# Kernel optimization log

Measured on AMD Instinct MI355X. Metric: run time of the kernel, lower is better.

Reference implementation:

```python
import jax, jax.numpy as jnp
import numpy as np

HEADS = 8
KEY_DIM = 64
GROUPS = 16
EPS = 1e-5


def setup_inputs() -> dict:
    key = jax.random.key(0)
    ks = jax.random.split(key, 7)
    b, c, h, w = 4, 256, 128, 128
    dk = KEY_DIM * HEADS  # 512
    x = jax.random.normal(ks[0], (b, c, h, w), dtype=jnp.float32)
    wq = jax.random.normal(ks[1], (dk, c), dtype=jnp.float32) * 0.02      # to_q (1x1, no bias)
    wkv = jax.random.normal(ks[2], (2 * dk, c), dtype=jnp.float32) * 0.02  # to_kv (1x1, no bias)
    wo = jax.random.normal(ks[3], (c, dk), dtype=jnp.float32) * 0.02       # to_out weight (1x1)
    bo = jax.random.normal(ks[4], (c,), dtype=jnp.float32) * 0.02          # to_out bias
    gamma = jnp.ones((2 * c,), dtype=jnp.float32)                          # GroupNorm weight
    beta = jnp.zeros((2 * c,), dtype=jnp.float32)                          # GroupNorm bias
    return {"x": x, "wq": wq, "wkv": wkv, "wo": wo, "bo": bo, "gamma": gamma, "beta": beta}


def reference(x, wq, wkv, wo, bo, gamma, beta):
    b, c, h, w = x.shape
    n = h * w
    xf = x.reshape(b, c, n)

    # 1x1 conv projections == channel GEMMs
    q = jnp.einsum('dc,bcn->bdn', wq, xf).reshape(b, HEADS, KEY_DIM, n)
    kv = jnp.einsum('dc,bcn->bdn', wkv, xf)
    k, v = jnp.split(kv, 2, axis=1)
    k = k.reshape(b, HEADS, KEY_DIM, n)
    v = v.reshape(b, HEADS, KEY_DIM, n)

    scale = KEY_DIM ** (-0.25)
    k = jax.nn.softmax(k * scale, axis=-1)   # softmax over spatial n
    q = jax.nn.softmax(q * scale, axis=-2)   # norm_queries: softmax over key_dim

    ctx = jnp.einsum('bhdn,bhen->bhde', k, v)   # [b,h,64,64]
    out = jnp.einsum('bhdn,bhde->bhen', q, ctx)  # [b,h,64,n]
    out = out.reshape(b, HEADS * KEY_DIM, n)

    out = jnp.einsum('od,bdn->bon', wo, out) + bo[None, :, None]  # to_out 1x1 conv

    y = jnp.concatenate([out, xf], axis=1)  # [b, 2c, n]
    c2 = 2 * c
    yg = y.reshape(b, GROUPS, (c2 // GROUPS) * n)
    mean = yg.mean(axis=2, keepdims=True)
    var = yg.var(axis=2, keepdims=True)
    yn = ((yg - mean) * jax.lax.rsqrt(var + EPS)).reshape(b, c2, n)
    yn = yn * gamma[None, :, None] + beta[None, :, None]
    return yn.reshape(b, c2, h, w)
```

## Files before the change

kernel.cpp:

```cpp
#include <hip/hip_runtime.h>

typedef int    i32x4 __attribute__((ext_vector_type(4)));
typedef float  f32x4 __attribute__((ext_vector_type(4)));
typedef __bf16 bf16x8 __attribute__((ext_vector_type(8)));
union B16 { i32x4 i; bf16x8 v; };

#define NN 16384
#define QSCALE 0.35355339059327373f
#define EPSV 1e-5f
#define GRPN 524288.0f

#define GSUM_OFF 0
#define GSQ_OFF  64
#define WS_ZERO_FLOATS 128


__device__ __forceinline__ ushort f2bfu(float f) {
  union { __bf16 h; ushort u; } c; c.h = (__bf16)f; return c.u;
}
__device__ __forceinline__ uint packbf2(float lo, float hi) {
  return (uint)f2bfu(lo) | ((uint)f2bfu(hi) << 16);
}
__device__ __forceinline__ void gload_lds16(const void* g, void* l) {
  __builtin_amdgcn_global_load_lds(
      (const __attribute__((address_space(1))) void*)g,
      (__attribute__((address_space(3))) void*)l, 16, 0, 0);
}

__global__ __launch_bounds__(256) void k_cvt3(const float* __restrict__ a,
                                              const float* __restrict__ bsrc,
                                              const float* __restrict__ c,
                                              ushort* __restrict__ d) {
  int i = (blockIdx.x * 256 + threadIdx.x) * 4;
  const float* s; int off;
  if (i < 131072)      { s = a;    off = 0; }
  else if (i < 393216) { s = bsrc; off = 131072; }
  else                 { s = c;    off = 393216; }
  float4 v = *(const float4*)(s + (i - off));
  uint2 p; p.x = packbf2(v.x, v.y); p.y = packbf2(v.z, v.w);
  *(uint2*)(d + i) = p;
}

__global__ __launch_bounds__(256) void k0_xprep(const float* __restrict__ x,
                                                float* __restrict__ outp,
                                                float* ws) {
  const int t = threadIdx.x;
  const int n0 = blockIdx.x * 64, b = blockIdx.z;
  __shared__ __align__(16) uint tile[64 * 130];
  const int cl = t >> 3;
  const int nb = (t & 7) * 8;
  const bool even = ((t >> 3) & 1) == 0;
  const int cpl = t >> 4;

  float4 va[8][2];
  #pragma unroll
  for (int cg = 0; cg < 8; ++cg) {
    const float* src = x + ((size_t)(b * 256 + cg * 32 + cl)) * NN + n0 + nb;
    va[cg][0] = *(const float4*)src;
    va[cg][1] = *(const float4*)(src + 4);
  }

  float s[8], s2[8];
  #pragma unroll
  for (int g = 0; g < 8; ++g) { s[g] = 0.f; s2[g] = 0.f; }

  #pragma unroll
  for (int cg = 0; cg < 8; ++cg) {
    float v[8] = {va[cg][0].x, va[cg][0].y, va[cg][0].z, va[cg][0].w,
                  va[cg][1].x, va[cg][1].y, va[cg][1].z, va[cg][1].w};
    #pragma unroll
    for (int j = 0; j < 8; ++j) { s[cg] += v[j]; s2[cg] += v[j] * v[j]; }
    float th[8];
    #pragma unroll
    for (int j = 0; j < 8; ++j) th[j] = __shfl_xor(v[j], 8);
    const int col = cg * 16 + cpl;
    #pragma unroll
    for (int jj = 0; jj < 4; ++jj) {
      const int j = even ? jj : (4 + jj);
      const float lo = even ? v[j] : th[j];
      const float hi = even ? th[j] : v[j];
      tile[(nb + j) * 130 + col] = packbf2(lo, hi);
    }
  }
  __syncthreads();
  {
    ushort* xT = (ushort*)(outp + ((size_t)(b * 512 + 256)) * NN);
    const int slot = t & 31;
    #pragma unroll
    for (int p = 0; p < 8; ++p) {
      const int n = p * 8 + (t >> 5);
      const uint* tp = &tile[n * 130 + slot * 4];
      i32x4 pk; pk[0] = (int)tp[0]; pk[1] = (int)tp[1]; pk[2] = (int)tp[2]; pk[3] = (int)tp[3];
      *(i32x4*)(xT + (size_t)(n0 + n) * 256 + slot * 8) = pk;
    }
  }
  #pragma unroll
  for (int g = 0; g < 8; ++g)
    #pragma unroll
    for (int m = 1; m <= 32; m <<= 1) {
      s[g] += __shfl_xor(s[g], m); s2[g] += __shfl_xor(s2[g], m);
    }
  __shared__ float rs[4][8], rq[4][8];
  const int w = t >> 6;
  if ((t & 63) == 0)
    #pragma unroll
    for (int g = 0; g < 8; ++g) { rs[w][g] = s[g]; rq[w][g] = s2[g]; }
  __syncthreads();
  if (t < 8) {
    atomicAdd(&ws[GSUM_OFF + b * 16 + 8 + t], rs[0][t] + rs[1][t] + rs[2][t] + rs[3][t]);
    atomicAdd(&ws[GSQ_OFF  + b * 16 + 8 + t], rq[0][t] + rq[1][t] + rq[2][t] + rq[3][t]);
  }
}

__global__ __launch_bounds__(512)
__attribute__((amdgpu_waves_per_eu(2, 2)))
void k1_kvctx(const float* outp,
              const ushort* __restrict__ wkv_bf,
              float* __restrict__ ctxpA,
              float* __restrict__ ctxpB,
              float* __restrict__ ksump) {
  const int t = threadIdx.x, lane = t & 63, w = t >> 6;
  const int l15 = lane & 15, l4 = lane >> 4;
  const int chunk = blockIdx.x, hq = blockIdx.y, b = blockIdx.z;
  const ushort* xT = (const ushort*)(outp + ((size_t)(b * 512 + 256)) * NN);
  __shared__ __align__(16) ushort xt[2][16384];
  __shared__ __align__(16) ushort kvb[2][8192];

  const int nbase = chunk * 512;

  auto STAGE = [&](ushort* bufp, int st) {
    #pragma unroll
    for (int j = 0; j < 4; ++j) {
      const int rl = w * 8 + j * 2 + (lane >> 5);
      const int slot = (lane & 31) ^ (rl & 31);
      const ushort* gp = xT + (size_t)(nbase + st * 64 + rl) * 256 + slot * 8;
      gload_lds16(gp, bufp + (w * 8 + j * 2) * 256);
    }
  };

  STAGE(xt[0], 0);

  const int rbase0 = (w < 4) ? (16 * w) : (512 + 16 * (w - 4));
  B16 afr[4][8];
  #pragma unroll
  for (int hi = 0; hi < 4; ++hi) {
    const int h = hq * 4 + hi;
    const ushort* wr = wkv_bf + (size_t)(rbase0 + h * 64 + l15) * 256 + l4 * 8;
    #pragma unroll
    for (int ks = 0; ks < 8; ++ks) afr[hi][ks].i = *(const i32x4*)(wr + ks * 32);
  }
  #pragma unroll
  for (int hi = 0; hi < 4; ++hi)
    #pragma unroll
    for (int ks = 0; ks < 8; ++ks)
      asm volatile("" : "+v"(afr[hi][ks].i));

  f32x4 ctxc[4][2];
  #pragma unroll
  for (int hi = 0; hi < 4; ++hi)
    #pragma unroll
    for (int ct = 0; ct < 2; ++ct) ctxc[hi][ct] = f32x4{0.f, 0.f, 0.f, 0.f};
  float ksp[4] = {0.f, 0.f, 0.f, 0.f};

  asm volatile("s_waitcnt vmcnt(0)" ::: "memory");
  __builtin_amdgcn_s_barrier();

  const int kvrow = ((w < 4) ? 16 * w : 64 + 16 * (w - 4)) + l15;

  for (int st = 0; st < 8; ++st) {
    const int cur = st & 1;
    if (st < 7) {
      STAGE(xt[cur ^ 1], st + 1);
      asm volatile("s_waitcnt vmcnt(4)" ::: "memory");
    } else {
      asm volatile("s_waitcnt vmcnt(0)" ::: "memory");
    }
    __builtin_amdgcn_s_barrier();
    const ushort* xb = xt[cur];

    #pragma unroll
    for (int hp2 = 0; hp2 < 2; ++hp2) {
      f32x4 acc[2][4];
      #pragma unroll
      for (int hi2 = 0; hi2 < 2; ++hi2)
        #pragma unroll
        for (int ct = 0; ct < 4; ++ct) acc[hi2][ct] = f32x4{0.f, 0.f, 0.f, 0.f};
      #pragma unroll
      for (int ks = 0; ks < 8; ++ks) {
        B16 bfr[4];
        #pragma unroll
        for (int ct = 0; ct < 4; ++ct) {
          const int n = ct * 16 + l15;
          const int slot = (ks * 4 + l4) ^ (n & 31);
          bfr[ct].i = *(const i32x4*)((const char*)xb + n * 512 + slot * 16);
        }
        #pragma unroll
        for (int hi2 = 0; hi2 < 2; ++hi2)
          #pragma unroll
          for (int ct = 0; ct < 4; ++ct)
            acc[hi2][ct] = __builtin_amdgcn_mfma_f32_16x16x32_bf16(
                bfr[ct].v, afr[hp2 * 2 + hi2][ks].v, acc[hi2][ct], 0, 0, 0);
      }
      #pragma unroll
      for (int hi2 = 0; hi2 < 2; ++hi2) {
        char* kb = (char*)kvb[hi2];
        #pragma unroll
        for (int ct = 0; ct < 4; ++ct) {
          float v0 = acc[hi2][ct][0], v1 = acc[hi2][ct][1];
          float v2 = acc[hi2][ct][2], v3 = acc[hi2][ct][3];
          if (w < 4) {
            v0 = __expf(v0 * QSCALE); v1 = __expf(v1 * QSCALE);
            v2 = __expf(v2 * QSCALE); v3 = __expf(v3 * QSCALE);
            ksp[hp2 * 2 + hi2] += (v0 + v1) + (v2 + v3);
          }
          uint2 pk; pk.x = packbf2(v0, v1); pk.y = packbf2(v2, v3);
          const int nn0 = ct * 16 + l4 * 4;
          *(uint2*)(kb + kvrow * 128 + (((nn0 >> 3) ^ (kvrow & 7)) << 4) + (nn0 & 7) * 2) = pk;
        }
      }
      asm volatile("s_waitcnt lgkmcnt(0)" ::: "memory");
      __builtin_amdgcn_s_barrier();
      #pragma unroll
      for (int hi2 = 0; hi2 < 2; ++hi2) {
        const char* kb = (const char*)kvb[hi2];
        #pragma unroll
        for (int ks = 0; ks < 2; ++ks) {
          const int ar = 16 * (w & 3) + l15;
          B16 a;
          a.i = *(const i32x4*)(kb + ar * 128 + (((ks * 4 + l4) ^ (ar & 7)) << 4));
          #pragma unroll
          for (int ct = 0; ct < 2; ++ct) {
            const int br = 64 + (w >> 2) * 32 + ct * 16 + l15;
            B16 bb;
            bb.i = *(const i32x4*)(kb + br * 128 + (((ks * 4 + l4) ^ (br & 7)) << 4));
            ctxc[hp2 * 2 + hi2][ct] = __builtin_amdgcn_mfma_f32_16x16x32_bf16(
                a.v, bb.v, ctxc[hp2 * 2 + hi2][ct], 0, 0, 0);
          }
        }
      }
      asm volatile("s_waitcnt lgkmcnt(0)" ::: "memory");
      __builtin_amdgcn_s_barrier();
    }
  }

  if (w < 4) {
    #pragma unroll
    for (int hi = 0; hi < 4; ++hi) {
      float s = ksp[hi];
      s += __shfl_xor(s, 16);
      s += __shfl_xor(s, 32);
      if (lane < 16)
        ksump[chunk * 2048 + (b * 8 + hq * 4 + hi) * 64 + 16 * w + l15] = s;
    }
  }
  float* base = (chunk < 16 ? ctxpA : ctxpB) + (size_t)(chunk & 15) * 131072;
  #pragma unroll
  for (int hi = 0; hi < 4; ++hi) {
    float* cp = base + (size_t)(b * 8 + hq * 4 + hi) * 4096;
    #pragma unroll
    for (int ct = 0; ct < 2; ++ct)
      #pragma unroll
      for (int r = 0; r < 4; ++r)
        cp[(16 * (w & 3) + l4 * 4 + r) * 64 + (w >> 2) * 32 + ct * 16 + l15] = ctxc[hi][ct][r];
  }
}

__global__ __launch_bounds__(256) void k1b_weff(const float* __restrict__ ctxpA,
                                                const float* __restrict__ ctxpB,
                                                const float* __restrict__ ksump,
                                                const ushort* __restrict__ wo_bf,
                                                ushort* __restrict__ weff_bf) {
  const int t = threadIdx.x, lane = t & 63, w = t >> 6;
  const int l15 = lane & 15, l4 = lane >> 4;
  const int h = blockIdx.x, b = blockIdx.y;
  __shared__ float ksinv[64];
  __shared__ __align__(16) float ctxs[64 * 68];
  if (t < 64) {
    float s = 0.f;
    #pragma unroll
    for (int c = 0; c < 32; ++c) s += ksump[c * 2048 + (b * 8 + h) * 64 + t];
    ksinv[t] = 1.f / s;
  }
  const int off = (b * 8 + h) * 4096;
  for (int i = t; i < 4096; i += 256) {
    float s = 0.f;
    #pragma unroll
    for (int c = 0; c < 16; ++c) s += ctxpA[(size_t)c * 131072 + off + i];
    #pragma unroll
    for (int c = 0; c < 16; ++c) s += ctxpB[(size_t)c * 131072 + off + i];
    ctxs[(i >> 6) * 68 + (i & 63)] = s;
  }
  __syncthreads();
  f32x4 acc[4][4];
  #pragma unroll
  for (int m = 0; m < 4; ++m)
    #pragma unroll
    for (int ct = 0; ct < 4; ++ct) acc[m][ct] = f32x4{0.f, 0.f, 0.f, 0.f};
  #pragma unroll
  for (int ks = 0; ks < 2; ++ks) {
    B16 bfr[4];
    #pragma unroll
    for (int ct = 0; ct < 4; ++ct) {
      const int d = ct * 16 + l15;
      const float inv = ksinv[d];
      const float* bp = &ctxs[d * 68 + ks * 32 + l4 * 8];
      #pragma unroll
      for (int j = 0; j < 4; ++j) {
        bfr[ct].v[j] = (__bf16)(bp[j] * inv);
        bfr[ct].v[4 + j] = (__bf16)(bp[4 + j] * inv);
      }
    }
    #pragma unroll
    for (int m = 0; m < 4; ++m) {
      B16 af;
      af.i = *(const i32x4*)(wo_bf + (size_t)(w * 64 + m * 16 + l15) * 512 + h * 64 + ks * 32 + l4 * 8);
      #pragma unroll
      for (int ct = 0; ct < 4; ++ct)
        acc[m][ct] = __builtin_amdgcn_mfma_f32_16x16x32_bf16(af.v, bfr[ct].v, acc[m][ct], 0, 0, 0);
    }
  }
  #pragma unroll
  for (int m = 0; m < 4; ++m)
    #pragma unroll
    for (int ct = 0; ct < 4; ++ct)
      #pragma unroll
      for (int r = 0; r < 4; ++r)
        weff_bf[((size_t)b * 256 + w * 64 + m * 16 + l4 * 4 + r) * 512 + h * 64 + ct * 16 + l15]
            = f2bfu(acc[m][ct][r]);
}

__global__ __launch_bounds__(256, 2) void k2_qy(float* outp,
                                                const ushort* __restrict__ wq_bf,
                                                const ushort* __restrict__ weff_bf,
                                                const float* __restrict__ bo,
                                                float* ws) {
  const int t = threadIdx.x, lane = t & 63, w = t >> 6;
  const int l15 = lane & 15, l4 = lane >> 4;
  const int n0 = blockIdx.x * 64, b = blockIdx.y;
  const ushort* xT = (const ushort*)(outp + ((size_t)(b * 512 + 256)) * NN);
  __shared__ __align__(16) ushort xt[64 * 256];
  __shared__ __align__(16) ushort PT[64 * 256];
  __shared__ float rsum[4][2], rsq[4][2];
  {
    #pragma unroll
    for (int j = 0; j < 8; ++j) {
      const int rl = w * 16 + j * 2 + (lane >> 5);
      const int slot = (lane & 31) ^ (rl & 31);
      const ushort* gp = xT + (size_t)(n0 + rl) * 256 + slot * 8;
      gload_lds16(gp, xt + (w * 16 + j * 2) * 256);
    }
    asm volatile("s_waitcnt vmcnt(0)" ::: "memory");
    __builtin_amdgcn_s_barrier();
  }
  f32x4 yacc[4][4];
  #pragma unroll
  for (int m = 0; m < 4; ++m)
    #pragma unroll
    for (int ct = 0; ct < 4; ++ct) yacc[m][ct] = f32x4{0.f, 0.f, 0.f, 0.f};

  for (int hp = 0; hp < 2; ++hp) {
    const int h = hp * 4 + w;
    f32x4 qacc[4][4];
    #pragma unroll
    for (int mt = 0; mt < 4; ++mt)
      #pragma unroll
      for (int ct = 0; ct < 4; ++ct) qacc[mt][ct] = f32x4{0.f, 0.f, 0.f, 0.f};
    #pragma unroll 2
    for (int ks = 0; ks < 8; ++ks) {
      B16 bfr[4];
      #pragma unroll
      for (int ct = 0; ct < 4; ++ct) {
        const int n = ct * 16 + l15;
        const int slot = (ks * 4 + l4) ^ (n & 31);
        bfr[ct].i = *(const i32x4*)((const char*)xt + n * 512 + slot * 16);
      }
      #pragma unroll
      for (int mt = 0; mt < 4; ++mt) {
        B16 af;
        af.i = *(const i32x4*)(wq_bf + (size_t)(h * 64 + mt * 16 + l15) * 256 + ks * 32 + l4 * 8);
        #pragma unroll
        for (int ct = 0; ct < 4; ++ct)
          qacc[mt][ct] = __builtin_amdgcn_mfma_f32_16x16x32_bf16(af.v, bfr[ct].v, qacc[mt][ct], 0, 0, 0);
      }
    }
    #pragma unroll
    for (int ct = 0; ct < 4; ++ct) {
      float sv[4][4]; float mx = -1e30f;
      #pragma unroll
      for (int mt = 0; mt < 4; ++mt)
        #pragma unroll
        for (int r = 0; r < 4; ++r) {
          sv[mt][r] = qacc[mt][ct][r] * QSCALE;
          mx = fmaxf(mx, sv[mt][r]);
        }
      mx = fmaxf(mx, __shfl_xor(mx, 16)); mx = fmaxf(mx, __shfl_xor(mx, 32));
      float ssum = 0.f;
      #pragma unroll
      for (int mt = 0; mt < 4; ++mt)
        #pragma unroll
        for (int r = 0; r < 4; ++r) { sv[mt][r] = __expf(sv[mt][r] - mx); ssum += sv[mt][r]; }
      ssum += __shfl_xor(ssum, 16); ssum += __shfl_xor(ssum, 32);
      const float inv = 1.f / ssum;
      const int n = ct * 16 + l15;
      #pragma unroll
      for (int mt = 0; mt < 4; ++mt)
        #pragma unroll
        for (int rp = 0; rp < 2; ++rp) {
          const uint pk = packbf2(sv[mt][2 * rp] * inv, sv[mt][2 * rp + 1] * inv);
          const int hd = w * 64 + mt * 16 + l4 * 4 + 2 * rp;
          *(uint*)((char*)PT + ((n * 512 + hd * 2) ^ ((n & 31) << 4))) = pk;
        }
    }
    __syncthreads();
    #pragma unroll 2
    for (int ks = 0; ks < 8; ++ks) {
      B16 bfr[4];
      #pragma unroll
      for (int ct = 0; ct < 4; ++ct) {
        const int n = ct * 16 + l15;
        const int slot = (ks * 4 + l4) ^ (n & 31);
        bfr[ct].i = *(const i32x4*)((const char*)PT + n * 512 + slot * 16);
      }
      #pragma unroll
      for (int m = 0; m < 4; ++m) {
        B16 af;
        af.i = *(const i32x4*)(weff_bf + ((size_t)b * 256 + w * 64 + m * 16 + l15) * 512
                               + hp * 256 + ks * 32 + l4 * 8);
        #pragma unroll
        for (int ct = 0; ct < 4; ++ct)
          yacc[m][ct] = __builtin_amdgcn_mfma_f32_16x16x32_bf16(af.v, bfr[ct].v, yacc[m][ct], 0, 0, 0);
      }
    }
    __syncthreads();
  }
  float sg[2] = {0.f, 0.f}, qg[2] = {0.f, 0.f};
  #pragma unroll
  for (int m = 0; m < 4; ++m) {
    const int o = w * 64 + m * 16 + l4 * 4;
    const f32x4 bv = *(const f32x4*)(bo + o);
    const int gi = m >> 1;
    #pragma unroll
    for (int ct = 0; ct < 4; ++ct)
      #pragma unroll
      for (int r = 0; r < 4; ++r) {
        const float val = yacc[m][ct][r] + bv[r];
        yacc[m][ct][r] = val;
        sg[gi] += val; qg[gi] += val * val;
      }
  }
  #pragma unroll
  for (int msk = 1; msk <= 32; msk <<= 1) {
    sg[0] += __shfl_xor(sg[0], msk); sg[1] += __shfl_xor(sg[1], msk);
    qg[0] += __shfl_xor(qg[0], msk); qg[1] += __shfl_xor(qg[1], msk);
  }
  if (lane == 0) { rsum[w][0] = sg[0]; rsum[w][1] = sg[1]; rsq[w][0] = qg[0]; rsq[w][1] = qg[1]; }
  __syncthreads();
  if (t < 8) {
    atomicAdd(&ws[GSUM_OFF + b * 16 + t], rsum[t >> 1][t & 1]);
    atomicAdd(&ws[GSQ_OFF + b * 16 + t], rsq[t >> 1][t & 1]);
  }
  #pragma unroll
  for (int m = 0; m < 4; ++m)
    #pragma unroll
    for (int ct = 0; ct < 4; ++ct)
      #pragma unroll
      for (int r = 0; r < 4; ++r)
        outp[((size_t)(b * 512) + w * 64 + m * 16 + l4 * 4 + r) * NN + n0 + ct * 16 + l15]
            = yacc[m][ct][r];
}

__global__ __launch_bounds__(256) void k3_groupnorm(
    const float* __restrict__ x, const float* __restrict__ gamma,
    const float* __restrict__ beta, const float* __restrict__ ws,
    float* out) {
  const int t = threadIdx.x;
  const int b = blockIdx.z, ch = blockIdx.y;
  const int n0 = blockIdx.x * 1024 + t * 4;
  const int g = ch >> 5;
  const float s = ws[GSUM_OFF + b * 16 + g];
  const float s2 = ws[GSQ_OFF + b * 16 + g];
  const float mean = s / GRPN;
  const float var = s2 / GRPN - mean * mean;
  const float inv = rsqrtf(var + EPSV);
  const float ga = gamma[ch] * inv;
  const float be = beta[ch] - mean * ga;
  float* op = out + ((size_t)(b * 512) + ch) * NN + n0;
  float4 v;
  if (ch < 256) v = *(const float4*)op;
  else v = *(const float4*)(x + ((size_t)(b * 256) + (ch - 256)) * NN + n0);
  v.x = v.x * ga + be;
  v.y = v.y * ga + be;
  v.z = v.z * ga + be;
  v.w = v.w * ga + be;
  *(float4*)op = v;
}

extern "C" void kernel_launch(void* const* d_in, const int* in_sizes, int n_in,
                              void* d_out, int out_size, void* d_ws, size_t ws_size,
                              hipStream_t stream) {
  const float* x     = (const float*)d_in[0];
  const float* wq    = (const float*)d_in[1];
  const float* wkv   = (const float*)d_in[2];
  const float* wo    = (const float*)d_in[3];
  const float* bo    = (const float*)d_in[4];
  const float* gamma = (const float*)d_in[5];
  const float* beta  = (const float*)d_in[6];
  float* out = (float*)d_out;
  float* ws = (float*)d_ws;

  float* spare0 = out + (size_t)256 * NN;
  ushort* wq_bf   = (ushort*)(spare0 + 2097152);
  ushort* wkv_bf  = wq_bf + 131072;
  ushort* wo_bf   = wkv_bf + 262144;
  ushort* weff_bf = wo_bf + 131072;
  float*  ksump   = (float*)(weff_bf + 524288);
  float*  ctxpA   = out + (size_t)(2 * 512 + 256) * NN + 2097152;
  float*  ctxpB   = out + (size_t)(3 * 512 + 256) * NN + 2097152;

  hipMemsetAsync(ws, 0, WS_ZERO_FLOATS * sizeof(float), stream);
  k_cvt3<<<512, 256, 0, stream>>>(wq, wkv, wo, wq_bf);
  k0_xprep<<<dim3(256, 1, 4), 256, 0, stream>>>(x, out, ws);
  k1_kvctx<<<dim3(32, 2, 4), 512, 0, stream>>>(out, wkv_bf, ctxpA, ctxpB, ksump);
  k1b_weff<<<dim3(8, 4), 256, 0, stream>>>(ctxpA, ctxpB, ksump, wo_bf, weff_bf);
  k2_qy<<<dim3(256, 4), 256, 0, stream>>>(out, wq_bf, weff_bf, bo, ws);
  k3_groupnorm<<<dim3(16, 512, 4), 256, 0, stream>>>(x, gamma, beta, ws, out);
}
```

Before: 244.4 us.

## Shrink k2_qy P tile to two heads per pass and raise occupancy

Result: slower. 287.9 us (+17.8%).

```diff
diff --git a/kernel.cpp b/kernel.cpp
--- a/kernel.cpp
+++ b/kernel.cpp
@@ -13,7 +13,6 @@
 #define GSUM_OFF 0
 #define GSQ_OFF  64
 #define WS_ZERO_FLOATS 128
-
 
 __device__ __forceinline__ ushort f2bfu(float f) {
   union { __bf16 h; ushort u; } c; c.h = (__bf16)f; return c.u;
@@ -329,7 +328,7 @@
             = f2bfu(acc[m][ct][r]);
 }
 
-__global__ __launch_bounds__(256, 2) void k2_qy(float* outp,
+__global__ __launch_bounds__(256, 3) void k2_qy(float* outp,
                                                 const ushort* __restrict__ wq_bf,
                                                 const ushort* __restrict__ weff_bf,
                                                 const float* __restrict__ bo,
@@ -339,7 +338,7 @@
   const int n0 = blockIdx.x * 64, b = blockIdx.y;
   const ushort* xT = (const ushort*)(outp + ((size_t)(b * 512 + 256)) * NN);
   __shared__ __align__(16) ushort xt[64 * 256];
-  __shared__ __align__(16) ushort PT[64 * 256];
+  __shared__ __align__(16) char PT[64 * 272];
   __shared__ float rsum[4][2], rsq[4][2];
   {
     #pragma unroll
@@ -358,39 +357,44 @@
     #pragma unroll
     for (int ct = 0; ct < 4; ++ct) yacc[m][ct] = f32x4{0.f, 0.f, 0.f, 0.f};
 
-  for (int hp = 0; hp < 2; ++hp) {
-    const int h = hp * 4 + w;
-    f32x4 qacc[4][4];
+  const int hw_lo = w & 1;
+  const int nh = w >> 1;
+
+  for (int hp2 = 0; hp2 < 4; ++hp2) {
+    const int h = hp2 * 2 + hw_lo;
+    f32x4 qacc[4][2];
     #pragma unroll
     for (int mt = 0; mt < 4; ++mt)
       #pragma unroll
-      for (int ct = 0; ct < 4; ++ct) qacc[mt][ct] = f32x4{0.f, 0.f, 0.f, 0.f};
-    #pragma unroll 2
+      for (int c2 = 0; c2 < 2; ++c2) qacc[mt][c2] = f32x4{0.f, 0.f, 0.f, 0.f};
+    __builtin_amdgcn_s_setprio(1);
+    #pragma unroll
     for (int ks = 0; ks < 8; ++ks) {
-      B16 bfr[4];
-      #pragma unroll
-      for (int ct = 0; ct < 4; ++ct) {
-        const int n = ct * 16 + l15;
+      B16 bfr[2];
+      #pragma unroll
+      for (int c2 = 0; c2 < 2; ++c2) {
+        const int n = nh * 32 + c2 * 16 + l15;
         const int slot = (ks * 4 + l4) ^ (n & 31);
-        bfr[ct].i = *(const i32x4*)((const char*)xt + n * 512 + slot * 16);
+        bfr[c2].i = *(const i32x4*)((const char*)xt + n * 512 + slot * 16);
       }
       #pragma unroll
       for (int mt = 0; mt < 4; ++mt) {
         B16 af;
         af.i = *(const i32x4*)(wq_bf + (size_t)(h * 64 + mt * 16 + l15) * 256 + ks * 32 + l4 * 8);
         #pragma unroll
-        for (int ct = 0; ct < 4; ++ct)
-          qacc[mt][ct] = __builtin_amdgcn_mfma_f32_16x16x32_bf16(af.v, bfr[ct].v, qacc[mt][ct], 0, 0, 0);
-      }
-    }
-    #pragma unroll
-    for (int ct = 0; ct < 4; ++ct) {
+        for (int c2 = 0; c2 < 2; ++c2)
+          qacc[mt][c2] = __builtin_amdgcn_mfma_f32_16x16x32_bf16(af.v, bfr[c2].v, qacc[mt][c2], 0, 0, 0);
+      }
+    }
+    __builtin_amdgcn_s_setprio(0);
+    #pragma unroll
+    for (int c2 = 0; c2 < 2; ++c2) {
       float sv[4][4]; float mx = -1e30f;
       #pragma unroll
       for (int mt = 0; mt < 4; ++mt)
         #pragma unroll
         for (int r = 0; r < 4; ++r) {
-          sv[mt][r] = qacc[mt][ct][r] * QSCALE;
+          sv[mt][r] = qacc[mt][c2][r] * QSCALE;
           mx = fmaxf(mx, sv[mt][r]);
         }
       mx = fmaxf(mx, __shfl_xor(mx, 16)); mx = fmaxf(mx, __shfl_xor(mx, 32));
@@ -401,37 +405,40 @@
         for (int r = 0; r < 4; ++r) { sv[mt][r] = __expf(sv[mt][r] - mx); ssum += sv[mt][r]; }
       ssum += __shfl_xor(ssum, 16); ssum += __shfl_xor(ssum, 32);
       const float inv = 1.f / ssum;
-      const int n = ct * 16 + l15;
+      const int n = nh * 32 + c2 * 16 + l15;
       #pragma unroll
       for (int mt = 0; mt < 4; ++mt)
         #pragma unroll
         for (int rp = 0; rp < 2; ++rp) {
           const uint pk = packbf2(sv[mt][2 * rp] * inv, sv[mt][2 * rp + 1] * inv);
-          const int hd = w * 64 + mt * 16 + l4 * 4 + 2 * rp;
-          *(uint*)((char*)PT + ((n * 512 + hd * 2) ^ ((n & 31) << 4))) = pk;
+          const int hd2 = hw_lo * 64 + mt * 16 + l4 * 4 + 2 * rp;
+          *(uint*)(PT + n * 272 + hd2 * 2) = pk;
         }
     }
-    __syncthreads();
-    #pragma unroll 2
-    for (int ks = 0; ks < 8; ++ks) {
+    asm volatile("s_waitcnt lgkmcnt(0)" ::: "memory");
+    __builtin_amdgcn_s_barrier();
+    __builtin_amdgcn_s_setprio(1);
+    #pragma unroll
+    for (int ks = 0; ks < 4; ++ks) {
       B16 bfr[4];
       #pragma unroll
       for (int ct = 0; ct < 4; ++ct) {
         const int n = ct * 16 + l15;
-        const int slot = (ks * 4 + l4) ^ (n & 31);
-        bfr[ct].i = *(const i32x4*)((const char*)PT + n * 512 + slot * 16);
+        bfr[ct].i = *(const i32x4*)(PT + n * 272 + ks * 64 + l4 * 16);
       }
       #pragma unroll
       for (int m = 0; m < 4; ++m) {
         B16 af;
         af.i = *(const i32x4*)(weff_bf + ((size_t)b * 256 + w * 64 + m * 16 + l15) * 512
-                               + hp * 256 + ks * 32 + l4 * 8);
+                               + hp2 * 128 + ks * 32 + l4 * 8);
         #pragma unroll
         for (int ct = 0; ct < 4; ++ct)
           yacc[m][ct] = __builtin_amdgcn_mfma_f32_16x16x32_bf16(af.v, bfr[ct].v, yacc[m][ct], 0, 0, 0);
       }
     }
-    __syncthreads();
+    __builtin_amdgcn_s_setprio(0);
+    asm volatile("s_waitcnt lgkmcnt(0)" ::: "memory");
+    __builtin_amdgcn_s_barrier();
   }
   float sg[2] = {0.f, 0.f}, qg[2] = {0.f, 0.f};
   #pragma unroll
```
